# Kernel optimization log

Measured on AMD Instinct MI355X. Metric: run time of the kernel, lower is better.

The kernel has to match this reference:

```python
import jax, jax.numpy as jnp
import numpy as np

B, A, D = 32, 1024, 128
THR = 0.05  # proximity_threshold


def setup_inputs() -> dict:
    key = jax.random.key(0)
    k1, k2, k3, k4, k5 = jax.random.split(key, 5)
    s = 1.0 / np.sqrt(D)
    return {
        "agent_embeds": jax.random.normal(k1, (B, A, D), jnp.float32),
        "agent_coords": jax.random.uniform(k2, (B, A, 2), jnp.float32),
        "agent_mask": jax.random.randint(k3, (B, A), 0, 2).astype(jnp.int32),
        "W1": (jax.random.normal(k4, (D, D), jnp.float32) * s),
        "b1": jnp.zeros((D,), jnp.float32),
        "W2": (jax.random.normal(k5, (D, D), jnp.float32) * s),
        "b2": jnp.zeros((D,), jnp.float32),
    }


def _cluster(coords, valid):
    """Greedy sequential proximity clustering (same order/semantics as the torch loop).
    coords [A,2], valid [A] bool -> assigned [A] int32 (group id; invalid agents = -2)."""
    diff = coords[:, None, :] - coords[None, :, :]          # [A,A,2]
    near_all = jnp.sum(diff * diff, axis=-1) < (THR * THR)   # dist < thr  <=>  dist^2 < thr^2
    assigned0 = jnp.where(valid, -1, -2).astype(jnp.int32)

    def step(carry, i):
        assigned, gid = carry
        start = assigned[i] == -1                 # valid and not yet assigned -> new group
        take = start & near_all[i] & (assigned == -1)  # includes i (dist ii = 0)
        assigned = jnp.where(take, gid, assigned)
        gid = gid + start.astype(jnp.int32)
        return (assigned, gid), None

    (assigned, _), _ = jax.lax.scan(step, (assigned0, jnp.int32(0)), jnp.arange(A))
    return assigned


def reference(agent_embeds, agent_coords, agent_mask, W1, b1, W2, b2):
    valid = agent_mask.astype(bool)                          # [B,A]
    assigned = jax.vmap(_cluster)(agent_coords, valid)       # [B,A] int32

    w = valid.astype(agent_embeds.dtype)                     # [B,A]
    seg = jnp.where(valid, assigned, 0)                      # invalid -> seg 0 with weight 0

    def pool(emb, sg, wt):  # per batch: segment-mean into at most A groups (padded)
        sums = jax.ops.segment_sum(emb * wt[:, None], sg, num_segments=A)  # [A,D]
        cnt = jax.ops.segment_sum(wt, sg, num_segments=A)                  # [A]
        return sums / jnp.maximum(cnt, 1.0)[:, None], cnt > 0

    group_tokens, group_mask = jax.vmap(pool)(agent_embeds, seg, w)  # [B,A,D], [B,A]

    # group_proj MLP applied to the whole (zero-padded) token tensor, as in torch
    h = jax.nn.gelu(group_tokens @ W1 + b1, approximate=False)
    group_tokens = h @ W2 + b2

    agent_to_group = jnp.where(valid, assigned, -1)
    return group_tokens, group_mask, agent_to_group
```

## Files before the change

### kernel.cpp

```cpp
#include <hip/hip_runtime.h>
#include <hip/hip_bf16.h>

#define NB 32
#define NA 1024
#define ND 128
#define TG 16

__device__ __forceinline__ float gelu_exact(float x) {
    return 0.5f * x * (1.0f + erff(x * 0.7071067811865476f));
}

__device__ __forceinline__ float dist2(float ax, float ay, float bx, float by) {
    float dx = ax - bx, dy = ay - by;
    return __fadd_rn(__fmul_rn(dx, dx), __fmul_rn(dy, dy));
}

__global__ __launch_bounds__(1024, 1) void fused_kernel(
    const float2* __restrict__ coords, const int* __restrict__ mask,
    const float* __restrict__ emb,
    int* __restrict__ gcount, float* __restrict__ tokens,
    float* __restrict__ out_mask, float* __restrict__ out_a2g,
    const float* __restrict__ b1, const float* __restrict__ W2,
    const float* __restrict__ b2, float* __restrict__ empty_row)
{
    __shared__ float2 ring[NA];
    __shared__ int cnt_s[NA];
    __shared__ int bufA[NA];
    __shared__ int bufB[NA];
    __shared__ int memb[NA];
    __shared__ int done_s[16];
    __shared__ int lead_cnt;

    const int tid = threadIdx.x;

    if (blockIdx.x == NB) {
        float* hbuf = (float*)ring;
        if (tid < ND) hbuf[tid] = gelu_exact(b1[tid]);
        __syncthreads();
        if (tid < ND) {
            float acc = b2[tid];
            for (int k = 0; k < ND; ++k) acc += hbuf[k] * W2[k * ND + tid];
            empty_row[tid] = acc;
        }
        return;
    }

    const int b = blockIdx.x;
    const int w = tid >> 6;
    const int lane = tid & 63;

    if (tid < 16) done_s[tid] = -1;
    if (tid == 0) lead_cnt = 0;

    float2 p = coords[(b << 10) + tid];
    const bool valid = mask[(b << 10) + tid] != 0;
    int asg = valid ? -1 : -2;
    bool alive = valid;
    const float thr2 = 0.05f * 0.05f;

    __syncthreads();

    int seen = 0;
    int target = (w == 0) ? 0 : -1;

    while (true) {
        int c = __hip_atomic_load(&lead_cnt, __ATOMIC_ACQUIRE,
                                  __HIP_MEMORY_SCOPE_WORKGROUP);
        if (c > seen) {
            do {
                float2 l = ring[seen];
                float d2 = dist2(p.x, p.y, l.x, l.y);
                if (alive && d2 < thr2) { asg = seen; alive = false; }
                ++seen;
            } while (seen < c);
            continue;
        }
        if (target < 0)
            target = __hip_atomic_load(&done_s[w - 1], __ATOMIC_ACQUIRE,
                                       __HIP_MEMORY_SCOPE_WORKGROUP);
        if (target >= 0 && seen >= target) break;
        __builtin_amdgcn_s_sleep(1);
    }

    __builtin_amdgcn_s_setprio(1);
    int pend = 0;
    unsigned long long bal;
    while ((bal = __ballot(alive)) != 0ULL) {
        const int L = (int)__builtin_ctzll(bal);
        const float lx = __builtin_bit_cast(float,
            __builtin_amdgcn_readlane(__builtin_bit_cast(int, p.x), L));
        const float ly = __builtin_bit_cast(float,
            __builtin_amdgcn_readlane(__builtin_bit_cast(int, p.y), L));
        float d2 = dist2(p.x, p.y, lx, ly);
        bool take = alive && (d2 < thr2);
        if (take) { asg = seen; alive = false; }
        if (lane == 0) ring[seen] = make_float2(lx, ly);
        ++seen;
        if (++pend == 8) {
            if (lane == 0)
                __hip_atomic_store(&lead_cnt, seen, __ATOMIC_RELEASE,
                                   __HIP_MEMORY_SCOPE_WORKGROUP);
            pend = 0;
        }
    }
    if (lane == 0) {
        __hip_atomic_store(&lead_cnt, seen, __ATOMIC_RELEASE,
                           __HIP_MEMORY_SCOPE_WORKGROUP);
        __hip_atomic_store(&done_s[w], seen, __ATOMIC_RELEASE,
                           __HIP_MEMORY_SCOPE_WORKGROUP);
    }
    __builtin_amdgcn_s_setprio(0);

    __syncthreads();
    const int G = lead_cnt;

    cnt_s[tid] = 0;
    __syncthreads();
    if (asg >= 0) atomicAdd(&cnt_s[asg], 1);
    __syncthreads();

    bufA[tid] = cnt_s[tid];
    __syncthreads();
    int* src = bufA;
    int* dst = bufB;
    for (int d = 1; d < NA; d <<= 1) {
        int v = src[tid];
        if (tid >= d) v += src[tid - d];
        dst[tid] = v;
        __syncthreads();
        int* tswap = src; src = dst; dst = tswap;
    }
    const int excl = src[tid] - cnt_s[tid];
    bufB[tid] = excl;
    bufA[tid] = excl;
    __syncthreads();
    if (asg >= 0) {
        int ppos = atomicAdd(&bufA[asg], 1);
        memb[ppos] = tid;
    }
    __syncthreads();

    out_a2g[(b << 10) + tid] = (asg == -2) ? -1.0f : (float)asg;
    out_mask[(b << 10) + tid] = (tid < G) ? 1.0f : 0.0f;
    if (tid == 0) gcount[b] = G;

    const int Gpad = (G + TG - 1) & ~(TG - 1);
    const float* eb = emb + ((size_t)(b) << 10) * ND;
    float* tb = tokens + ((size_t)(b) << 10) * ND;
    for (int g = w; g < Gpad; g += 16) {
        float a0 = 0.0f, a1 = 0.0f;
        if (g < G) {
            const int n = cnt_s[g];
            const int off = bufB[g];
            for (int k = 0; k < n; ++k) {
                const int a = memb[off + k];
                const float* ea = eb + (size_t)a * ND;
                a0 += ea[lane];
                a1 += ea[lane + 64];
            }
            const float den = fmaxf((float)n, 1.0f);
            a0 /= den; a1 /= den;
        }
        tb[(size_t)g * ND + lane] = a0;
        tb[(size_t)g * ND + lane + 64] = a1;
    }
}

__global__ __launch_bounds__(256, 2) void mlp_kernel(
    const float* __restrict__ tokens, const int* __restrict__ gcount,
    const float* __restrict__ empty_row,
    const float4* __restrict__ W1, const float* __restrict__ b1,
    const float4* __restrict__ W2, const float* __restrict__ b2,
    float* __restrict__ out0)
{
    const int b = blockIdx.y;
    const int g0 = blockIdx.x * TG;
    const int tid = threadIdx.x;
    float* ob = out0 + ((size_t)(b << 10) + g0) * ND;

    if (g0 >= gcount[b]) {
        float4 r = ((const float4*)empty_row)[tid & 31];
        float4* ob4 = (float4*)ob;
        ob4[tid] = r;
        ob4[tid + 256] = r;
        return;
    }

    __shared__ float4 Wl[4096];
    __shared__ float tok[TG][ND];

    {
        const float4* tsrc = (const float4*)(tokens + ((size_t)(b << 10) + g0) * ND);
        float4* tdst = (float4*)&tok[0][0];
        tdst[tid] = tsrc[tid];
        tdst[tid + 256] = tsrc[tid + 256];
    }
#pragma unroll
    for (int i = 0; i < 16; ++i) Wl[tid + i * 256] = W1[tid + i * 256];
    __syncthreads();

    const int jq = tid & 31;
    const int gs = tid >> 5;
    float acc[2][4];
#pragma unroll
    for (int jj = 0; jj < 4; ++jj) { acc[0][jj] = 0.0f; acc[1][jj] = 0.0f; }

#pragma unroll 4
    for (int dd = 0; dd < ND; ++dd) {
        float4 wv = Wl[dd * 32 + jq];
        float t0 = tok[gs][dd];
        float t1 = tok[gs + 8][dd];
        acc[0][0] += t0 * wv.x; acc[0][1] += t0 * wv.y;
        acc[0][2] += t0 * wv.z; acc[0][3] += t0 * wv.w;
        acc[1][0] += t1 * wv.x; acc[1][1] += t1 * wv.y;
        acc[1][2] += t1 * wv.z; acc[1][3] += t1 * wv.w;
    }
    float4 bb = ((const float4*)b1)[jq];
    __syncthreads();
    {
        float4 h;
        h.x = gelu_exact(acc[0][0] + bb.x);
        h.y = gelu_exact(acc[0][1] + bb.y);
        h.z = gelu_exact(acc[0][2] + bb.z);
        h.w = gelu_exact(acc[0][3] + bb.w);
        *(float4*)&tok[gs][jq * 4] = h;
        h.x = gelu_exact(acc[1][0] + bb.x);
        h.y = gelu_exact(acc[1][1] + bb.y);
        h.z = gelu_exact(acc[1][2] + bb.z);
        h.w = gelu_exact(acc[1][3] + bb.w);
        *(float4*)&tok[gs + 8][jq * 4] = h;
    }
#pragma unroll
    for (int i = 0; i < 16; ++i) Wl[tid + i * 256] = W2[tid + i * 256];
    __syncthreads();

#pragma unroll
    for (int jj = 0; jj < 4; ++jj) { acc[0][jj] = 0.0f; acc[1][jj] = 0.0f; }
#pragma unroll 4
    for (int dd = 0; dd < ND; ++dd) {
        float4 wv = Wl[dd * 32 + jq];
        float t0 = tok[gs][dd];
        float t1 = tok[gs + 8][dd];
        acc[0][0] += t0 * wv.x; acc[0][1] += t0 * wv.y;
        acc[0][2] += t0 * wv.z; acc[0][3] += t0 * wv.w;
        acc[1][0] += t1 * wv.x; acc[1][1] += t1 * wv.y;
        acc[1][2] += t1 * wv.z; acc[1][3] += t1 * wv.w;
    }
    float4 cbv = ((const float4*)b2)[jq];
    {
        float4 o;
        o.x = acc[0][0] + cbv.x; o.y = acc[0][1] + cbv.y;
        o.z = acc[0][2] + cbv.z; o.w = acc[0][3] + cbv.w;
        *(float4*)&ob[(size_t)gs * ND + jq * 4] = o;
        o.x = acc[1][0] + cbv.x; o.y = acc[1][1] + cbv.y;
        o.z = acc[1][2] + cbv.z; o.w = acc[1][3] + cbv.w;
        *(float4*)&ob[(size_t)(gs + 8) * ND + jq * 4] = o;
    }
}

extern "C" void kernel_launch(void* const* d_in, const int* in_sizes, int n_in,
                              void* d_out, int out_size, void* d_ws, size_t ws_size,
                              hipStream_t stream) {
    const float* emb    = (const float*)d_in[0];
    const float* coords = (const float*)d_in[1];
    const int*   mask   = (const int*)d_in[2];
    const float* W1     = (const float*)d_in[3];
    const float* b1     = (const float*)d_in[4];
    const float* W2     = (const float*)d_in[5];
    const float* b2     = (const float*)d_in[6];

    float* out0 = (float*)d_out;
    float* out1 = out0 + (size_t)NB * NA * ND;
    float* out2 = out1 + (size_t)NB * NA;

    float* ws_tok   = (float*)d_ws;
    int*   ws_gcnt  = (int*)(ws_tok + (size_t)NB * NA * ND);
    float* ws_empty = (float*)(ws_gcnt + NB);

    fused_kernel<<<NB + 1, 1024, 0, stream>>>(
        (const float2*)coords, mask, emb,
        ws_gcnt, ws_tok, out1, out2,
        b1, W2, b2, ws_empty);
    mlp_kernel<<<dim3(NA / TG, NB), 256, 0, stream>>>(
        ws_tok, ws_gcnt, ws_empty,
        (const float4*)W1, b1, (const float4*)W2, b2, out0);
}
```

Before: 154.6 us.

## Split pooling out of cluster kernel into grid-wide atomic segment-sum

```diff
diff --git a/kernel.cpp b/kernel.cpp
--- a/kernel.cpp
+++ b/kernel.cpp
@@ -15,19 +15,15 @@
     return __fadd_rn(__fmul_rn(dx, dx), __fmul_rn(dy, dy));
 }
 
-__global__ __launch_bounds__(1024, 1) void fused_kernel(
+__global__ __launch_bounds__(1024, 1) void cluster_kernel(
     const float2* __restrict__ coords, const int* __restrict__ mask,
-    const float* __restrict__ emb,
-    int* __restrict__ gcount, float* __restrict__ tokens,
+    int* __restrict__ assigned, int* __restrict__ gcount,
+    float* __restrict__ sums, float* __restrict__ counts,
     float* __restrict__ out_mask, float* __restrict__ out_a2g,
     const float* __restrict__ b1, const float* __restrict__ W2,
     const float* __restrict__ b2, float* __restrict__ empty_row)
 {
     __shared__ float2 ring[NA];
-    __shared__ int cnt_s[NA];
-    __shared__ int bufA[NA];
-    __shared__ int bufB[NA];
-    __shared__ int memb[NA];
     __shared__ int done_s[16];
     __shared__ int lead_cnt;
 
@@ -64,26 +60,29 @@
     int target = (w == 0) ? 0 : -1;
 
     while (true) {
-        int c = __hip_atomic_load(&lead_cnt, __ATOMIC_ACQUIRE,
-                                  __HIP_MEMORY_SCOPE_WORKGROUP);
-        if (c > seen) {
-            do {
-                float2 l = ring[seen];
-                float d2 = dist2(p.x, p.y, l.x, l.y);
-                if (alive && d2 < thr2) { asg = seen; alive = false; }
-                ++seen;
-            } while (seen < c);
-            continue;
-        }
         if (target < 0)
             target = __hip_atomic_load(&done_s[w - 1], __ATOMIC_ACQUIRE,
                                        __HIP_MEMORY_SCOPE_WORKGROUP);
-        if (target >= 0 && seen >= target) break;
+        if (__ballot(alive) == 0ULL) {
+            if (target >= 0) { seen = target; break; }
+        } else {
+            int c = __hip_atomic_load(&lead_cnt, __ATOMIC_ACQUIRE,
+                                      __HIP_MEMORY_SCOPE_WORKGROUP);
+            if (c > seen) {
+                do {
+                    float2 l = ring[seen];
+                    float d2 = dist2(p.x, p.y, l.x, l.y);
+                    if (alive && d2 < thr2) { asg = seen; alive = false; }
+                    ++seen;
+                } while (seen < c);
+                continue;
+            }
+            if (target >= 0 && seen >= target) break;
+        }
         __builtin_amdgcn_s_sleep(1);
     }
 
     __builtin_amdgcn_s_setprio(1);
-    int pend = 0;
     unsigned long long bal;
     while ((bal = __ballot(alive)) != 0ULL) {
         const int L = (int)__builtin_ctzll(bal);
@@ -96,79 +95,60 @@
         if (take) { asg = seen; alive = false; }
         if (lane == 0) ring[seen] = make_float2(lx, ly);
         ++seen;
-        if (++pend == 8) {
-            if (lane == 0)
-                __hip_atomic_store(&lead_cnt, seen, __ATOMIC_RELEASE,
-                                   __HIP_MEMORY_SCOPE_WORKGROUP);
-            pend = 0;
-        }
-    }
-    if (lane == 0) {
-        __hip_atomic_store(&lead_cnt, seen, __ATOMIC_RELEASE,
-                           __HIP_MEMORY_SCOPE_WORKGROUP);
+        if (lane == 0)
+            __hip_atomic_store(&lead_cnt, seen, __ATOMIC_RELEASE,
+                               __HIP_MEMORY_SCOPE_WORKGROUP);
+    }
+    if (lane == 0)
         __hip_atomic_store(&done_s[w], seen, __ATOMIC_RELEASE,
                            __HIP_MEMORY_SCOPE_WORKGROUP);
-    }
     __builtin_amdgcn_s_setprio(0);
 
     __syncthreads();
     const int G = lead_cnt;
 
-    cnt_s[tid] = 0;
-    __syncthreads();
-    if (asg >= 0) atomicAdd(&cnt_s[asg], 1);
-    __syncthreads();
-
-    bufA[tid] = cnt_s[tid];
-    __syncthreads();
-    int* src = bufA;
-    int* dst = bufB;
-    for (int d = 1; d < NA; d <<= 1) {
-        int v = src[tid];
-        if (tid >= d) v += src[tid - d];
-        dst[tid] = v;
-        __syncthreads();
-        int* tswap = src; src = dst; dst = tswap;
-    }
-    const int excl = src[tid] - cnt_s[tid];
-    bufB[tid] = excl;
-    bufA[tid] = excl;
-    __syncthreads();
-    if (asg >= 0) {
-        int ppos = atomicAdd(&bufA[asg], 1);
-        memb[ppos] = tid;
-    }
-    __syncthreads();
-
+    assigned[(b << 10) + tid] = asg;
     out_a2g[(b << 10) + tid] = (asg == -2) ? -1.0f : (float)asg;
     out_mask[(b << 10) + tid] = (tid < G) ? 1.0f : 0.0f;
     if (tid == 0) gcount[b] = G;
 
     const int Gpad = (G + TG - 1) & ~(TG - 1);
-    const float* eb = emb + ((size_t)(b) << 10) * ND;
-    float* tb = tokens + ((size_t)(b) << 10) * ND;
-    for (int g = w; g < Gpad; g += 16) {
-        float a0 = 0.0f, a1 = 0.0f;
-        if (g < G) {
-            const int n = cnt_s[g];
-            const int off = bufB[g];
-            for (int k = 0; k < n; ++k) {
-                const int a = memb[off + k];
-                const float* ea = eb + (size_t)a * ND;
-                a0 += ea[lane];
-                a1 += ea[lane + 64];
-            }
-            const float den = fmaxf((float)n, 1.0f);
-            a0 /= den; a1 /= den;
-        }
-        tb[(size_t)g * ND + lane] = a0;
-        tb[(size_t)g * ND + lane + 64] = a1;
-    }
+    float4* s4 = (float4*)(sums + (((size_t)b) << 10) * ND);
+    for (int i = tid; i < Gpad * 32; i += 1024)
+        s4[i] = make_float4(0.f, 0.f, 0.f, 0.f);
+    if (tid < Gpad) counts[(b << 10) + tid] = 0.0f;
+}
+
+__global__ __launch_bounds__(256) void fill_kernel(
+    const float* __restrict__ empty_row, float4* __restrict__ out0)
+{
+    const int idx = blockIdx.x * 256 + threadIdx.x;
+    float4 r = ((const float4*)empty_row)[idx & 31];
+    out0[idx] = r;
+}
+
+__global__ __launch_bounds__(256) void pool_kernel(
+    const float4* __restrict__ emb, const int* __restrict__ assigned,
+    float* __restrict__ sums, float* __restrict__ counts)
+{
+    const int idx = blockIdx.x * 256 + threadIdx.x;
+    const int al = idx >> 5;
+    const int dq = idx & 31;
+    const int g = assigned[al];
+    if (g < 0) return;
+    const int b = al >> 10;
+    float4 e = emb[(size_t)al * 32 + dq];
+    float* s = sums + (((size_t)((b << 10) + g)) * ND) + dq * 4;
+    atomicAdd(s + 0, e.x);
+    atomicAdd(s + 1, e.y);
+    atomicAdd(s + 2, e.z);
+    atomicAdd(s + 3, e.w);
+    if (dq == 0) atomicAdd(&counts[(b << 10) + g], 1.0f);
 }
 
 __global__ __launch_bounds__(256, 2) void mlp_kernel(
-    const float* __restrict__ tokens, const int* __restrict__ gcount,
-    const float* __restrict__ empty_row,
+    const float* __restrict__ sums, const float* __restrict__ counts,
+    const int* __restrict__ gcount,
     const float4* __restrict__ W1, const float* __restrict__ b1,
     const float4* __restrict__ W2, const float* __restrict__ b2,
     float* __restrict__ out0)
@@ -176,24 +156,22 @@
     const int b = blockIdx.y;
     const int g0 = blockIdx.x * TG;
     const int tid = threadIdx.x;
+    if (g0 >= gcount[b]) return;
     float* ob = out0 + ((size_t)(b << 10) + g0) * ND;
-
-    if (g0 >= gcount[b]) {
-        float4 r = ((const float4*)empty_row)[tid & 31];
-        float4* ob4 = (float4*)ob;
-        ob4[tid] = r;
-        ob4[tid + 256] = r;
-        return;
-    }
 
     __shared__ float4 Wl[4096];
     __shared__ float tok[TG][ND];
 
     {
-        const float4* tsrc = (const float4*)(tokens + ((size_t)(b << 10) + g0) * ND);
+        const float4* s4 = (const float4*)(sums + ((size_t)(b << 10) + g0) * ND);
         float4* tdst = (float4*)&tok[0][0];
-        tdst[tid] = tsrc[tid];
-        tdst[tid + 256] = tsrc[tid + 256];
+#pragma unroll
+        for (int i = 0; i < 2; ++i) {
+            int l = tid + i * 256;
+            float c = fmaxf(counts[(b << 10) + g0 + (l >> 5)], 1.0f);
+            float4 v = s4[l];
+            tdst[l] = make_float4(v.x / c, v.y / c, v.z / c, v.w / c);
+        }
     }
 #pragma unroll
     for (int i = 0; i < 16; ++i) Wl[tid + i * 256] = W1[tid + i * 256];
@@ -273,15 +251,21 @@
     float* out1 = out0 + (size_t)NB * NA * ND;
     float* out2 = out1 + (size_t)NB * NA;
 
-    float* ws_tok   = (float*)d_ws;
-    int*   ws_gcnt  = (int*)(ws_tok + (size_t)NB * NA * ND);
-    float* ws_empty = (float*)(ws_gcnt + NB);
-
-    fused_kernel<<<NB + 1, 1024, 0, stream>>>(
-        (const float2*)coords, mask, emb,
-        ws_gcnt, ws_tok, out1, out2,
+    float* ws_sums   = (float*)d_ws;
+    float* ws_counts = ws_sums + (size_t)NB * NA * ND;
+    int*   ws_asg    = (int*)(ws_counts + (size_t)NB * NA);
+    int*   ws_gcnt   = ws_asg + (size_t)NB * NA;
+    float* ws_empty  = (float*)(ws_gcnt + NB);
+
+    cluster_kernel<<<NB + 1, 1024, 0, stream>>>(
+        (const float2*)coords, mask, ws_asg, ws_gcnt,
+        ws_sums, ws_counts, out1, out2,
         b1, W2, b2, ws_empty);
+    fill_kernel<<<NB * NA * 32 / 256, 256, 0, stream>>>(
+        ws_empty, (float4*)out0);
+    pool_kernel<<<NB * NA * 32 / 256, 256, 0, stream>>>(
+        (const float4*)emb, ws_asg, ws_sums, ws_counts);
     mlp_kernel<<<dim3(NA / TG, NB), 256, 0, stream>>>(
-        ws_tok, ws_gcnt, ws_empty,
+        ws_sums, ws_counts, ws_gcnt,
         (const float4*)W1, b1, (const float4*)W2, b2, out0);
 }
```

After: 170.9 us. 1.11x slower.
